# Kernel optimization log

Measured on AMD Instinct MI355X. Metric: run time of the kernel, lower is better.

## Reference

```python
import jax, jax.numpy as jnp
import numpy as np

N = 100000       # nodes
E = 800000       # edges (avg degree 8)
D_IN = 256
D_H = 128
K = 16           # cluster_num
LAMBDA1 = 1.0    # args.alphaH
LAMBDA2 = 0.5    # args.alphaO
GAMMA = 0.1      # args.step_size_gamma


def setup_inputs() -> dict:
    key = jax.random.key(0)
    ks = jax.random.split(key, 8)
    x = jax.random.normal(ks[0], (N, D_IN), jnp.float32)
    edge_index = jax.random.randint(ks[1], (2, E), 0, N, jnp.int32)
    # learned params (glorot-ish small init to keep Gram term numerically tame)
    W1 = jax.random.normal(ks[2], (D_IN, D_H), jnp.float32) * 0.002
    b1 = jnp.zeros((D_H,), jnp.float32)
    W2 = jax.random.normal(ks[3], (D_H, D_H), jnp.float32) * 0.01
    b2 = jnp.zeros((D_H,), jnp.float32)
    Wf = jax.random.normal(ks[4], (D_H, K), jnp.float32) * 0.05
    bf = jnp.zeros((K,), jnp.float32)
    return {"x": x, "edge_index": edge_index, "W1": W1, "b1": b1,
            "W2": W2, "b2": b2, "Wf": Wf, "bf": bf}


def _gcn_norm(edge_index, n):
    # add self loops, symmetric normalization D^-1/2 A D^-1/2 (PyG gcn_norm)
    loops = jnp.arange(n, dtype=edge_index.dtype)
    row = jnp.concatenate([edge_index[0], loops])   # source
    col = jnp.concatenate([edge_index[1], loops])   # target
    w = jnp.ones(row.shape[0], jnp.float32)
    deg = jax.ops.segment_sum(w, col, num_segments=n)
    dinv = jnp.where(deg > 0, jax.lax.rsqrt(jnp.maximum(deg, 1.0)), 0.0)
    return row, col, dinv[row] * w * dinv[col]


def _deprop_layer(x, W, b, row, col, w, n):
    x = x @ W                                               # lin (no bias)
    z = (1.0 - GAMMA * LAMBDA1 + GAMMA * LAMBDA2) * x
    # propagate: gather source features, scale by edge weight, scatter-add to target
    s = GAMMA * LAMBDA1 * jax.ops.segment_sum(w[:, None] * x[row], col, num_segments=n)
    # dense Gram correction: x @ (x^T x), d_h x d_h contraction
    t = GAMMA * LAMBDA2 * (x @ (x.T @ x))
    return jax.nn.relu(z + s - t + b)                       # bias add + ReLU


def reference(x, edge_index, W1, b1, W2, b2, Wf, bf):
    n = x.shape[0]
    row, col, w = _gcn_norm(edge_index, n)  # cached=True -> computed once, reused
    x = _deprop_layer(x, W1, b1, row, col, w, n)
    x = _deprop_layer(x, W2, b2, row, col, w, n)
    logits = x @ Wf + bf                    # fc; dropout is identity in eval mode
    return jax.nn.log_softmax(logits, axis=1)
```

## Files before the change

kernel.cpp:

```cpp
#include <hip/hip_runtime.h>

#define NNODES 100000
#define NEDGES 800000
#define DIN    256
#define DH     128
#define KCLS   16
#define SCAN_NBLK 98
#define GCH 64
#define GRAM_BLK 256

typedef unsigned short u16;
typedef short s16x8 __attribute__((ext_vector_type(8)));
typedef float f32x4 __attribute__((ext_vector_type(4)));

static constexpr float CZ = 0.95f;
static constexpr float CS = 0.10f;
static constexpr float CT = 0.05f;

__device__ __forceinline__ u16 f2b(float f) {
    unsigned u = __builtin_bit_cast(unsigned, f);
    return (u16)((u + 0x7FFFu + ((u >> 16) & 1u)) >> 16);
}
__device__ __forceinline__ float b2f(u16 b) {
    return __builtin_bit_cast(float, ((unsigned)b) << 16);
}


__global__ __launch_bounds__(256) void zero_kernel(int* __restrict__ p) {
    int i = blockIdx.x * 256 + threadIdx.x;
    if (i < NNODES) p[i] = 0;
}

__global__ __launch_bounds__(256) void hist_kernel(const int* __restrict__ col, int* counts) {
    int i = blockIdx.x * 256 + threadIdx.x;
    if (i < NEDGES) atomicAdd(&counts[col[i]], 1);
}

__global__ __launch_bounds__(256) void dinv_kernel(const int* __restrict__ counts, float* dinv) {
    int i = blockIdx.x * 256 + threadIdx.x;
    if (i < NNODES) dinv[i] = rsqrtf((float)(counts[i] + 1));
}

__global__ __launch_bounds__(256) void scan1_kernel(const int* __restrict__ counts,
                                                    int* __restrict__ offsets, int* __restrict__ bsum) {
    __shared__ int ls[256];
    const int b = blockIdx.x, t = threadIdx.x;
    const int base = b * 1024 + t * 4;
    int v0 = (base + 0 < NNODES) ? counts[base + 0] : 0;
    int v1 = (base + 1 < NNODES) ? counts[base + 1] : 0;
    int v2 = (base + 2 < NNODES) ? counts[base + 2] : 0;
    int v3 = (base + 3 < NNODES) ? counts[base + 3] : 0;
    ls[t] = v0 + v1 + v2 + v3;
    __syncthreads();
    for (int off = 1; off < 256; off <<= 1) {
        int v = (t >= off) ? ls[t - off] : 0;
        __syncthreads();
        ls[t] += v;
        __syncthreads();
    }
    int excl = (t == 0) ? 0 : ls[t - 1];
    if (t == 255) bsum[b] = ls[255];
    if (base + 0 < NNODES) offsets[base + 0] = excl;
    if (base + 1 < NNODES) offsets[base + 1] = excl + v0;
    if (base + 2 < NNODES) offsets[base + 2] = excl + v0 + v1;
    if (base + 3 < NNODES) offsets[base + 3] = excl + v0 + v1 + v2;
}

__global__ __launch_bounds__(128) void scan2_kernel(int* bsum) {
    __shared__ int ls[128];
    const int t = threadIdx.x;
    int v = (t < SCAN_NBLK) ? bsum[t] : 0;
    ls[t] = v;
    __syncthreads();
    for (int off = 1; off < 128; off <<= 1) {
        int u = (t >= off) ? ls[t - off] : 0;
        __syncthreads();
        ls[t] += u;
        __syncthreads();
    }
    if (t < SCAN_NBLK) bsum[t] = ls[t] - v;
}

__global__ __launch_bounds__(256) void scan3_kernel(int* __restrict__ offsets, const int* __restrict__ bsum) {
    const int b = blockIdx.x, t = threadIdx.x;
    const int add = bsum[b];
    const int base = b * 1024 + t * 4;
    #pragma unroll
    for (int i = 0; i < 4; ++i)
        if (base + i < NNODES) offsets[base + i] += add;
    if (b == 0 && t == 0) offsets[NNODES] = NEDGES;
}

__global__ __launch_bounds__(256)
void fill_kernel(const int* __restrict__ row, const int* __restrict__ col,
                 const int* __restrict__ offsets, int* __restrict__ cursor,
                 int* __restrict__ eidx) {
    int e = blockIdx.x * 256 + threadIdx.x;
    if (e >= NEDGES) return;
    int c = col[e];
    int p = offsets[c] + atomicAdd(&cursor[c], 1);
    eidx[p] = row[e];
}

__global__ __launch_bounds__(256)
void gather_b(const u16* __restrict__ Hb, const float* __restrict__ dinv,
              const int* __restrict__ offsets, const int* __restrict__ eidx,
              u16* __restrict__ Sb) {
    const int t = threadIdx.x;
    const int grp = t >> 4;
    const int gl  = t & 15;
    const int node = blockIdx.x * 16 + grp;
    if (node >= NNODES) return;
    const s16x8* H8 = (const s16x8*)Hb;
    const float d = dinv[node];
    s16x8 hv = H8[(size_t)node * 16 + gl];
    float a[8];
    #pragma unroll
    for (int i = 0; i < 8; ++i) a[i] = d * d * b2f((u16)hv[i]);
    int p = offsets[node];
    const int e = offsets[node + 1];
    for (; p + 1 < e; p += 2) {
        int   r0 = eidx[p],  r1 = eidx[p + 1];
        float w0 = dinv[r0] * d, w1 = dinv[r1] * d;
        s16x8 h0 = H8[(size_t)r0 * 16 + gl];
        s16x8 h1 = H8[(size_t)r1 * 16 + gl];
        #pragma unroll
        for (int i = 0; i < 8; ++i) a[i] = fmaf(w0, b2f((u16)h0[i]), a[i]);
        #pragma unroll
        for (int i = 0; i < 8; ++i) a[i] = fmaf(w1, b2f((u16)h1[i]), a[i]);
    }
    if (p < e) {
        int   r0 = eidx[p];
        float w0 = dinv[r0] * d;
        s16x8 h0 = H8[(size_t)r0 * 16 + gl];
        #pragma unroll
        for (int i = 0; i < 8; ++i) a[i] = fmaf(w0, b2f((u16)h0[i]), a[i]);
    }
    s16x8 o;
    #pragma unroll
    for (int i = 0; i < 8; ++i) o[i] = (short)f2b(a[i]);
    ((s16x8*)Sb)[(size_t)node * 16 + gl] = o;
}


__global__ __launch_bounds__(256)
void cvt_x_kernel(const float* __restrict__ x, u16* __restrict__ xb) {
    const long total = (long)NNODES * DIN / 8;
    for (long i = blockIdx.x * 256L + threadIdx.x; i < total; i += (long)gridDim.x * 256) {
        const float4* p = (const float4*)&x[i * 8];
        float4 u0 = p[0], u1 = p[1];
        s16x8 v;
        v[0] = (short)f2b(u0.x); v[1] = (short)f2b(u0.y);
        v[2] = (short)f2b(u0.z); v[3] = (short)f2b(u0.w);
        v[4] = (short)f2b(u1.x); v[5] = (short)f2b(u1.y);
        v[6] = (short)f2b(u1.z); v[7] = (short)f2b(u1.w);
        *(s16x8*)&xb[i * 8] = v;
    }
}

template<int KD>
__global__ __launch_bounds__(256)
void tr_w_kernel(const float* __restrict__ W, u16* __restrict__ Wt) {
    int idx = blockIdx.x * 256 + threadIdx.x;
    if (idx < 128 * KD) {
        int c = idx / KD, k = idx % KD;
        Wt[idx] = f2b(W[k * 128 + c]);
    }
}

template<int KD, int EPI>
__global__ __launch_bounds__(256, 4)
void mm_bt(const u16* __restrict__ A, const u16* __restrict__ Bt,
           u16* __restrict__ Out, const u16* __restrict__ Hb,
           const u16* __restrict__ Sb, const float* __restrict__ bias,
           int nrows)
{
    __shared__ __align__(16) u16 as_[2][128 * 40];
    __shared__ __align__(16) u16 bs_[2][128 * 40];
    const int t = threadIdx.x;
    const int w = t >> 6, l = t & 63;
    const int l15 = l & 15, g = l >> 4;
    const int row0 = blockIdx.x * 128;

    const int sr = t >> 2, so = t & 3;
    int arow[2];
    arow[0] = min(row0 + sr,      nrows - 1);
    arow[1] = min(row0 + 64 + sr, nrows - 1);

    #pragma unroll
    for (int i = 0; i < 2; ++i) {
        s16x8 va = *(const s16x8*)&A [(size_t)arow[i] * KD + so * 8];
        s16x8 vb = *(const s16x8*)&Bt[(size_t)(sr + i * 64) * KD + so * 8];
        *(s16x8*)&as_[0][(sr + i * 64) * 40 + so * 8] = va;
        *(s16x8*)&bs_[0][(sr + i * 64) * 40 + so * 8] = vb;
    }
    __syncthreads();

    f32x4 acc[2][8] = {};
    constexpr int NK = KD / 32;

    for (int kc = 0; kc < NK; ++kc) {
        const int buf = kc & 1;
        s16x8 va[2], vb[2];
        const bool pf = (kc + 1 < NK);
        if (pf) {
            const int k0 = (kc + 1) * 32;
            #pragma unroll
            for (int i = 0; i < 2; ++i) {
                va[i] = *(const s16x8*)&A [(size_t)arow[i] * KD + k0 + so * 8];
                vb[i] = *(const s16x8*)&Bt[(size_t)(sr + i * 64) * KD + k0 + so * 8];
            }
        }
        s16x8 af0 = *(const s16x8*)&as_[buf][(w * 32 +      l15) * 40 + g * 8];
        s16x8 af1 = *(const s16x8*)&as_[buf][(w * 32 + 16 + l15) * 40 + g * 8];
        #pragma unroll
        for (int n = 0; n < 8; ++n) {
            s16x8 bfr = *(const s16x8*)&bs_[buf][(n * 16 + l15) * 40 + g * 8];
            acc[0][n] = __builtin_amdgcn_mfma_f32_16x16x32_bf16(af0, bfr, acc[0][n], 0, 0, 0);
            acc[1][n] = __builtin_amdgcn_mfma_f32_16x16x32_bf16(af1, bfr, acc[1][n], 0, 0, 0);
        }
        if (pf) {
            #pragma unroll
            for (int i = 0; i < 2; ++i) {
                *(s16x8*)&as_[buf ^ 1][(sr + i * 64) * 40 + so * 8] = va[i];
                *(s16x8*)&bs_[buf ^ 1][(sr + i * 64) * 40 + so * 8] = vb[i];
            }
        }
        __syncthreads();
    }

    float bv[8];
    if (EPI) {
        #pragma unroll
        for (int n = 0; n < 8; ++n) bv[n] = bias[n * 16 + l15];
    }
    #pragma unroll
    for (int m = 0; m < 2; ++m) {
        #pragma unroll
        for (int j = 0; j < 4; ++j) {
            int grow = row0 + w * 32 + m * 16 + g * 4 + j;
            if (grow < nrows) {
                size_t base = (size_t)grow * 128;
                #pragma unroll
                for (int n = 0; n < 8; ++n) {
                    int col = n * 16 + l15;
                    float v = acc[m][n][j];
                    if (EPI) {
                        float h = b2f(Hb[base + col]);
                        float s = b2f(Sb[base + col]);
                        v = fmaxf(CZ * h + CS * s - CT * v + bv[n], 0.f);
                    }
                    Out[base + col] = f2b(v);
                }
            }
        }
    }
}

__global__ __launch_bounds__(256)
void gram_mfma(const u16* __restrict__ Hb, float* __restrict__ P, int nrows)
{
    __shared__ __align__(16) u16 ht[2][128 * GCH];
    const int t = threadIdx.x;
    const int w = t >> 6, l = t & 63;
    const int l15 = l & 15, g = l >> 4;
    const int nch = (nrows + GCH - 1) / GCH;

    f32x4 acc[2][8] = {};

    const int sr = t >> 2, sq = t & 3;

    {
        int gr = blockIdx.x * GCH + sr;
        #pragma unroll
        for (int i4 = 0; i4 < 4; ++i4) {
            int c0 = sq * 32 + i4 * 8;
            s16x8 v = {};
            if (gr < nrows) v = *(const s16x8*)&Hb[(size_t)gr * DH + c0];
            #pragma unroll
            for (int i = 0; i < 8; ++i) {
                int c = c0 + i;
                ht[0][c * GCH + (sr ^ ((c & 7) << 3))] = (u16)v[i];
            }
        }
    }
    __syncthreads();

    int buf = 0;
    for (int ch = blockIdx.x; ch < nch; ch += gridDim.x, buf ^= 1) {
        int chn = ch + gridDim.x;
        if (chn < nch) {
            int gr = chn * GCH + sr;
            #pragma unroll
            for (int i4 = 0; i4 < 4; ++i4) {
                int c0 = sq * 32 + i4 * 8;
                s16x8 v = {};
                if (gr < nrows) v = *(const s16x8*)&Hb[(size_t)gr * DH + c0];
                #pragma unroll
                for (int i = 0; i < 8; ++i) {
                    int c = c0 + i;
                    ht[buf ^ 1][c * GCH + (sr ^ ((c & 7) << 3))] = (u16)v[i];
                }
            }
        }
        #pragma unroll
        for (int ks = 0; ks < 2; ++ks) {
            const int kx = (ks * 32 + g * 8) ^ ((l & 7) << 3);
            s16x8 a0 = *(const s16x8*)&ht[buf][(w * 32 +      l15) * GCH + kx];
            s16x8 a1 = *(const s16x8*)&ht[buf][(w * 32 + 16 + l15) * GCH + kx];
            #pragma unroll
            for (int n = 0; n < 8; ++n) {
                s16x8 bfr = *(const s16x8*)&ht[buf][(n * 16 + l15) * GCH + kx];
                acc[0][n] = __builtin_amdgcn_mfma_f32_16x16x32_bf16(a0, bfr, acc[0][n], 0, 0, 0);
                acc[1][n] = __builtin_amdgcn_mfma_f32_16x16x32_bf16(a1, bfr, acc[1][n], 0, 0, 0);
            }
        }
        __syncthreads();
    }

    float* Pb = P + (size_t)blockIdx.x * (DH * DH);
    #pragma unroll
    for (int m = 0; m < 2; ++m)
        #pragma unroll
        for (int j = 0; j < 4; ++j) {
            int prow = w * 32 + m * 16 + g * 4 + j;
            #pragma unroll
            for (int n = 0; n < 8; ++n)
                Pb[prow * DH + n * 16 + l15] = acc[m][n][j];
        }
}

__global__ __launch_bounds__(256)
void gram_reduce(const float* __restrict__ P, u16* __restrict__ Gb) {
    int idx = blockIdx.x * 256 + threadIdx.x;
    float s = 0.f;
    #pragma unroll 8
    for (int p = 0; p < GRAM_BLK; ++p)
        s += P[(size_t)p * (DH * DH) + idx];
    Gb[idx] = f2b(s);
}

__global__ __launch_bounds__(256)
void fc_mfma(const u16* __restrict__ Xb, const float* __restrict__ Wf,
             const float* __restrict__ bf, float* __restrict__ out, int nrows)
{
    __shared__ __align__(16) u16 wt[KCLS * DH];
    const int t = threadIdx.x;
    const int w = t >> 6, l = t & 63;
    const int l15 = l & 15, g = l >> 4;
    const int row0 = blockIdx.x * 128 + w * 32;

    for (int idx = t; idx < KCLS * DH; idx += 256) {
        int c = idx >> 7, k = idx & 127;
        wt[c * DH + (k ^ ((c & 7) << 3))] = f2b(Wf[k * KCLS + c]);
    }
    __syncthreads();

    int r[2];
    r[0] = min(row0 + l15,      nrows - 1);
    r[1] = min(row0 + 16 + l15, nrows - 1);

    f32x4 acc[2] = {};
    #pragma unroll
    for (int k0 = 0; k0 < DH; k0 += 32) {
        s16x8 a0 = *(const s16x8*)&Xb[(size_t)r[0] * DH + k0 + g * 8];
        s16x8 a1 = *(const s16x8*)&Xb[(size_t)r[1] * DH + k0 + g * 8];
        s16x8 bfr = *(const s16x8*)&wt[l15 * DH + ((k0 + g * 8) ^ ((l & 7) << 3))];
        acc[0] = __builtin_amdgcn_mfma_f32_16x16x32_bf16(a0, bfr, acc[0], 0, 0, 0);
        acc[1] = __builtin_amdgcn_mfma_f32_16x16x32_bf16(a1, bfr, acc[1], 0, 0, 0);
    }

    const float bias = bf[l15];
    #pragma unroll
    for (int m = 0; m < 2; ++m) {
        #pragma unroll
        for (int j = 0; j < 4; ++j) {
            int grow = row0 + m * 16 + g * 4 + j;
            float v = acc[m][j] + bias;
            float mx = v;
            #pragma unroll
            for (int o = 8; o >= 1; o >>= 1)
                mx = fmaxf(mx, __shfl_xor(mx, o));
            float e = expf(v - mx);
            float ssum = e;
            #pragma unroll
            for (int o = 8; o >= 1; o >>= 1)
                ssum += __shfl_xor(ssum, o);
            if (grow < nrows)
                out[(size_t)grow * KCLS + l15] = v - mx - logf(ssum);
        }
    }
}

extern "C" void kernel_launch(void* const* d_in, const int* in_sizes, int n_in,
                              void* d_out, int out_size, void* d_ws, size_t ws_size,
                              hipStream_t stream) {
    const float* x  = (const float*)d_in[0];
    const int*   ei = (const int*)d_in[1];
    const float* W1 = (const float*)d_in[2];
    const float* b1 = (const float*)d_in[3];
    const float* W2 = (const float*)d_in[4];
    const float* b2 = (const float*)d_in[5];
    const float* Wf = (const float*)d_in[6];
    const float* bf = (const float*)d_in[7];
    float* out = (float*)d_out;

    const int* row = ei;
    const int* col = ei + NEDGES;

    float* dinv    = (float*)d_ws;
    float* P       = dinv + 102400;
    int*   counts  = (int*)(P + (size_t)GRAM_BLK * DH * DH);
    int*   offsets = counts + 102400;
    int*   bsum    = offsets + 102656;
    int*   eidx    = bsum + 128;
    u16*   B0b     = (u16*)(eidx + NEDGES);
    u16*   xb      = B0b + (size_t)NNODES * DH;
    u16*   B1b     = xb;
    u16*   Sb      = xb + (size_t)NNODES * DH;
    u16*   W1t     = xb + (size_t)NNODES * DIN;
    u16*   W2t     = W1t + 128 * DIN;
    u16*   Gb      = W2t + 128 * DH;

    dim3 b256(256);
    const int gN  = (NNODES + 255) / 256;
    const int gE  = (NEDGES + 255) / 256;
    const int gMM = (NNODES + 127) / 128;
    const int gGA = (NNODES + 15) / 16;

    zero_kernel<<<gN, b256, 0, stream>>>(counts);
    hist_kernel<<<gE, b256, 0, stream>>>(col, counts);
    dinv_kernel<<<gN, b256, 0, stream>>>(counts, dinv);
    scan1_kernel<<<SCAN_NBLK, b256, 0, stream>>>(counts, offsets, bsum);
    scan2_kernel<<<1, 128, 0, stream>>>(bsum);
    scan3_kernel<<<SCAN_NBLK, b256, 0, stream>>>(offsets, bsum);
    zero_kernel<<<gN, b256, 0, stream>>>(counts);
    fill_kernel<<<gE, b256, 0, stream>>>(row, col, offsets, counts, eidx);
    cvt_x_kernel<<<2048, b256, 0, stream>>>(x, xb);
    tr_w_kernel<DIN><<<(128 * DIN + 255) / 256, b256, 0, stream>>>(W1, W1t);
    tr_w_kernel<DH><<<(128 * DH + 255) / 256, b256, 0, stream>>>(W2, W2t);

    mm_bt<DIN, 0><<<gMM, b256, 0, stream>>>(xb, W1t, B0b, nullptr, nullptr, nullptr, NNODES);
    gram_mfma<<<GRAM_BLK, b256, 0, stream>>>(B0b, P, NNODES);
    gram_reduce<<<64, b256, 0, stream>>>(P, Gb);
    gather_b<<<gGA, b256, 0, stream>>>(B0b, dinv, offsets, eidx, Sb);
    mm_bt<DH, 1><<<gMM, b256, 0, stream>>>(B0b, Gb, B1b, B0b, Sb, b1, NNODES);

    mm_bt<DH, 0><<<gMM, b256, 0, stream>>>(B1b, W2t, B0b, nullptr, nullptr, nullptr, NNODES);
    gram_mfma<<<GRAM_BLK, b256, 0, stream>>>(B0b, P, NNODES);
    gram_reduce<<<64, b256, 0, stream>>>(P, Gb);
    gather_b<<<gGA, b256, 0, stream>>>(B0b, dinv, offsets, eidx, Sb);
    mm_bt<DH, 1><<<gMM, b256, 0, stream>>>(B0b, Gb, B1b, B0b, Sb, b2, NNODES);

    fc_mfma<<<gMM, b256, 0, stream>>>(B1b, Wf, bf, out, NNODES);
}
```

Before: 334.0 us.

## Fuse fp32-to-bf16 conversion into first GEMM and co-launch Gram with gather

The standalone cvt_x pass is removed, so the first mm_bt reads fp32 x directly and converts it to bf16 while loading tiles. This avoids writing and re-reading a bf16 copy of x, at the price of twice the bytes per A-tile load inside the GEMM. The Gram partial-product kernel and the neighbour gather kernel are also merged into one launch, with the first 256 blocks doing Gram and the rest doing gather. This lets the two independent stages run side by side and fill the GPU, but it makes the block types within one kernel uneven in work. Workspace buffers are relaid out now that xb is gone.

```diff
diff --git a/kernel.cpp b/kernel.cpp
--- a/kernel.cpp
+++ b/kernel.cpp
@@ -23,6 +23,14 @@
 }
 __device__ __forceinline__ float b2f(u16 b) {
     return __builtin_bit_cast(float, ((unsigned)b) << 16);
+}
+__device__ __forceinline__ s16x8 f2b8(float4 u0, float4 u1) {
+    s16x8 v;
+    v[0] = (short)f2b(u0.x); v[1] = (short)f2b(u0.y);
+    v[2] = (short)f2b(u0.z); v[3] = (short)f2b(u0.w);
+    v[4] = (short)f2b(u1.x); v[5] = (short)f2b(u1.y);
+    v[6] = (short)f2b(u1.z); v[7] = (short)f2b(u1.w);
+    return v;
 }
 
 
@@ -102,61 +110,6 @@
     eidx[p] = row[e];
 }
 
-__global__ __launch_bounds__(256)
-void gather_b(const u16* __restrict__ Hb, const float* __restrict__ dinv,
-              const int* __restrict__ offsets, const int* __restrict__ eidx,
-              u16* __restrict__ Sb) {
-    const int t = threadIdx.x;
-    const int grp = t >> 4;
-    const int gl  = t & 15;
-    const int node = blockIdx.x * 16 + grp;
-    if (node >= NNODES) return;
-    const s16x8* H8 = (const s16x8*)Hb;
-    const float d = dinv[node];
-    s16x8 hv = H8[(size_t)node * 16 + gl];
-    float a[8];
-    #pragma unroll
-    for (int i = 0; i < 8; ++i) a[i] = d * d * b2f((u16)hv[i]);
-    int p = offsets[node];
-    const int e = offsets[node + 1];
-    for (; p + 1 < e; p += 2) {
-        int   r0 = eidx[p],  r1 = eidx[p + 1];
-        float w0 = dinv[r0] * d, w1 = dinv[r1] * d;
-        s16x8 h0 = H8[(size_t)r0 * 16 + gl];
-        s16x8 h1 = H8[(size_t)r1 * 16 + gl];
-        #pragma unroll
-        for (int i = 0; i < 8; ++i) a[i] = fmaf(w0, b2f((u16)h0[i]), a[i]);
-        #pragma unroll
-        for (int i = 0; i < 8; ++i) a[i] = fmaf(w1, b2f((u16)h1[i]), a[i]);
-    }
-    if (p < e) {
-        int   r0 = eidx[p];
-        float w0 = dinv[r0] * d;
-        s16x8 h0 = H8[(size_t)r0 * 16 + gl];
-        #pragma unroll
-        for (int i = 0; i < 8; ++i) a[i] = fmaf(w0, b2f((u16)h0[i]), a[i]);
-    }
-    s16x8 o;
-    #pragma unroll
-    for (int i = 0; i < 8; ++i) o[i] = (short)f2b(a[i]);
-    ((s16x8*)Sb)[(size_t)node * 16 + gl] = o;
-}
-
-
-__global__ __launch_bounds__(256)
-void cvt_x_kernel(const float* __restrict__ x, u16* __restrict__ xb) {
-    const long total = (long)NNODES * DIN / 8;
-    for (long i = blockIdx.x * 256L + threadIdx.x; i < total; i += (long)gridDim.x * 256) {
-        const float4* p = (const float4*)&x[i * 8];
-        float4 u0 = p[0], u1 = p[1];
-        s16x8 v;
-        v[0] = (short)f2b(u0.x); v[1] = (short)f2b(u0.y);
-        v[2] = (short)f2b(u0.z); v[3] = (short)f2b(u0.w);
-        v[4] = (short)f2b(u1.x); v[5] = (short)f2b(u1.y);
-        v[6] = (short)f2b(u1.z); v[7] = (short)f2b(u1.w);
-        *(s16x8*)&xb[i * 8] = v;
-    }
-}
 
 template<int KD>
 __global__ __launch_bounds__(256)
@@ -168,9 +121,9 @@
     }
 }
 
-template<int KD, int EPI>
+template<int KD, int EPI, int AF>
 __global__ __launch_bounds__(256, 4)
-void mm_bt(const u16* __restrict__ A, const u16* __restrict__ Bt,
+void mm_bt(const void* __restrict__ Avoid, const u16* __restrict__ Bt,
            u16* __restrict__ Out, const u16* __restrict__ Hb,
            const u16* __restrict__ Sb, const float* __restrict__ bias,
            int nrows)
@@ -182,6 +135,9 @@
     const int l15 = l & 15, g = l >> 4;
     const int row0 = blockIdx.x * 128;
 
+    const u16*   Ab = (const u16*)Avoid;
+    const float* Af = (const float*)Avoid;
+
     const int sr = t >> 2, so = t & 3;
     int arow[2];
     arow[0] = min(row0 + sr,      nrows - 1);
@@ -189,7 +145,13 @@
 
     #pragma unroll
     for (int i = 0; i < 2; ++i) {
-        s16x8 va = *(const s16x8*)&A [(size_t)arow[i] * KD + so * 8];
+        s16x8 va;
+        if (AF) {
+            const float4* p = (const float4*)&Af[(size_t)arow[i] * KD + so * 8];
+            va = f2b8(p[0], p[1]);
+        } else {
+            va = *(const s16x8*)&Ab[(size_t)arow[i] * KD + so * 8];
+        }
         s16x8 vb = *(const s16x8*)&Bt[(size_t)(sr + i * 64) * KD + so * 8];
         *(s16x8*)&as_[0][(sr + i * 64) * 40 + so * 8] = va;
         *(s16x8*)&bs_[0][(sr + i * 64) * 40 + so * 8] = vb;
@@ -207,7 +169,12 @@
             const int k0 = (kc + 1) * 32;
             #pragma unroll
             for (int i = 0; i < 2; ++i) {
-                va[i] = *(const s16x8*)&A [(size_t)arow[i] * KD + k0 + so * 8];
+                if (AF) {
+                    const float4* p = (const float4*)&Af[(size_t)arow[i] * KD + k0 + so * 8];
+                    va[i] = f2b8(p[0], p[1]);
+                } else {
+                    va[i] = *(const s16x8*)&Ab[(size_t)arow[i] * KD + k0 + so * 8];
+                }
                 vb[i] = *(const s16x8*)&Bt[(size_t)(sr + i * 64) * KD + k0 + so * 8];
             }
         }
@@ -258,39 +225,24 @@
 }
 
 __global__ __launch_bounds__(256)
-void gram_mfma(const u16* __restrict__ Hb, float* __restrict__ P, int nrows)
+void gram_gather(const u16* __restrict__ Hb, const float* __restrict__ dinv,
+                 const int* __restrict__ offsets, const int* __restrict__ eidx,
+                 float* __restrict__ P, u16* __restrict__ Sb, int nrows)
 {
     __shared__ __align__(16) u16 ht[2][128 * GCH];
     const int t = threadIdx.x;
-    const int w = t >> 6, l = t & 63;
-    const int l15 = l & 15, g = l >> 4;
-    const int nch = (nrows + GCH - 1) / GCH;
-
-    f32x4 acc[2][8] = {};
-
-    const int sr = t >> 2, sq = t & 3;
-
-    {
-        int gr = blockIdx.x * GCH + sr;
-        #pragma unroll
-        for (int i4 = 0; i4 < 4; ++i4) {
-            int c0 = sq * 32 + i4 * 8;
-            s16x8 v = {};
-            if (gr < nrows) v = *(const s16x8*)&Hb[(size_t)gr * DH + c0];
-            #pragma unroll
-            for (int i = 0; i < 8; ++i) {
-                int c = c0 + i;
-                ht[0][c * GCH + (sr ^ ((c & 7) << 3))] = (u16)v[i];
-            }
-        }
-    }
-    __syncthreads();
-
-    int buf = 0;
-    for (int ch = blockIdx.x; ch < nch; ch += gridDim.x, buf ^= 1) {
-        int chn = ch + gridDim.x;
-        if (chn < nch) {
-            int gr = chn * GCH + sr;
+
+    if (blockIdx.x < GRAM_BLK) {
+        const int bid = blockIdx.x;
+        const int w = t >> 6, l = t & 63;
+        const int l15 = l & 15, g = l >> 4;
+        const int nch = (nrows + GCH - 1) / GCH;
+
+        f32x4 acc[2][8] = {};
+        const int sr = t >> 2, sq = t & 3;
+
+        {
+            int gr = bid * GCH + sr;
             #pragma unroll
             for (int i4 = 0; i4 < 4; ++i4) {
                 int c0 = sq * 32 + i4 * 8;
@@ -299,35 +251,89 @@
                 #pragma unroll
                 for (int i = 0; i < 8; ++i) {
                     int c = c0 + i;
-                    ht[buf ^ 1][c * GCH + (sr ^ ((c & 7) << 3))] = (u16)v[i];
+                    ht[0][c * GCH + (sr ^ ((c & 7) << 3))] = (u16)v[i];
                 }
             }
         }
-        #pragma unroll
-        for (int ks = 0; ks < 2; ++ks) {
-            const int kx = (ks * 32 + g * 8) ^ ((l & 7) << 3);
-            s16x8 a0 = *(const s16x8*)&ht[buf][(w * 32 +      l15) * GCH + kx];
-            s16x8 a1 = *(const s16x8*)&ht[buf][(w * 32 + 16 + l15) * GCH + kx];
-            #pragma unroll
-            for (int n = 0; n < 8; ++n) {
-                s16x8 bfr = *(const s16x8*)&ht[buf][(n * 16 + l15) * GCH + kx];
-                acc[0][n] = __builtin_amdgcn_mfma_f32_16x16x32_bf16(a0, bfr, acc[0][n], 0, 0, 0);
-                acc[1][n] = __builtin_amdgcn_mfma_f32_16x16x32_bf16(a1, bfr, acc[1][n], 0, 0, 0);
-            }
-        }
-        __syncthreads();
-    }
-
-    float* Pb = P + (size_t)blockIdx.x * (DH * DH);
-    #pragma unroll
-    for (int m = 0; m < 2; ++m)
-        #pragma unroll
-        for (int j = 0; j < 4; ++j) {
-            int prow = w * 32 + m * 16 + g * 4 + j;
-            #pragma unroll
-            for (int n = 0; n < 8; ++n)
-                Pb[prow * DH + n * 16 + l15] = acc[m][n][j];
-        }
+        __syncthreads();
+
+        int buf = 0;
+        for (int ch = bid; ch < nch; ch += GRAM_BLK, buf ^= 1) {
+            int chn = ch + GRAM_BLK;
+            if (chn < nch) {
+                int gr = chn * GCH + sr;
+                #pragma unroll
+                for (int i4 = 0; i4 < 4; ++i4) {
+                    int c0 = sq * 32 + i4 * 8;
+                    s16x8 v = {};
+                    if (gr < nrows) v = *(const s16x8*)&Hb[(size_t)gr * DH + c0];
+                    #pragma unroll
+                    for (int i = 0; i < 8; ++i) {
+                        int c = c0 + i;
+                        ht[buf ^ 1][c * GCH + (sr ^ ((c & 7) << 3))] = (u16)v[i];
+                    }
+                }
+            }
+            #pragma unroll
+            for (int ks = 0; ks < 2; ++ks) {
+                const int kx = (ks * 32 + g * 8) ^ ((l & 7) << 3);
+                s16x8 a0 = *(const s16x8*)&ht[buf][(w * 32 +      l15) * GCH + kx];
+                s16x8 a1 = *(const s16x8*)&ht[buf][(w * 32 + 16 + l15) * GCH + kx];
+                #pragma unroll
+                for (int n = 0; n < 8; ++n) {
+                    s16x8 bfr = *(const s16x8*)&ht[buf][(n * 16 + l15) * GCH + kx];
+                    acc[0][n] = __builtin_amdgcn_mfma_f32_16x16x32_bf16(a0, bfr, acc[0][n], 0, 0, 0);
+                    acc[1][n] = __builtin_amdgcn_mfma_f32_16x16x32_bf16(a1, bfr, acc[1][n], 0, 0, 0);
+                }
+            }
+            __syncthreads();
+        }
+
+        float* Pb = P + (size_t)bid * (DH * DH);
+        #pragma unroll
+        for (int m = 0; m < 2; ++m)
+            #pragma unroll
+            for (int j = 0; j < 4; ++j) {
+                int prow = w * 32 + m * 16 + g * 4 + j;
+                #pragma unroll
+                for (int n = 0; n < 8; ++n)
+                    Pb[prow * DH + n * 16 + l15] = acc[m][n][j];
+            }
+    } else {
+        const int grp = t >> 4;
+        const int gl  = t & 15;
+        const int node = (blockIdx.x - GRAM_BLK) * 16 + grp;
+        if (node >= NNODES) return;
+        const s16x8* H8 = (const s16x8*)Hb;
+        const float d = dinv[node];
+        s16x8 hv = H8[(size_t)node * 16 + gl];
+        float a[8];
+        #pragma unroll
+        for (int i = 0; i < 8; ++i) a[i] = d * d * b2f((u16)hv[i]);
+        int p = offsets[node];
+        const int e = offsets[node + 1];
+        for (; p + 1 < e; p += 2) {
+            int   r0 = eidx[p],  r1 = eidx[p + 1];
+            float w0 = dinv[r0] * d, w1 = dinv[r1] * d;
+            s16x8 h0 = H8[(size_t)r0 * 16 + gl];
+            s16x8 h1 = H8[(size_t)r1 * 16 + gl];
+            #pragma unroll
+            for (int i = 0; i < 8; ++i) a[i] = fmaf(w0, b2f((u16)h0[i]), a[i]);
+            #pragma unroll
+            for (int i = 0; i < 8; ++i) a[i] = fmaf(w1, b2f((u16)h1[i]), a[i]);
+        }
+        if (p < e) {
+            int   r0 = eidx[p];
+            float w0 = dinv[r0] * d;
+            s16x8 h0 = H8[(size_t)r0 * 16 + gl];
+            #pragma unroll
+            for (int i = 0; i < 8; ++i) a[i] = fmaf(w0, b2f((u16)h0[i]), a[i]);
+        }
+        s16x8 o;
+        #pragma unroll
+        for (int i = 0; i < 8; ++i) o[i] = (short)f2b(a[i]);
+        ((s16x8*)Sb)[(size_t)node * 16 + gl] = o;
+    }
 }
 
 __global__ __launch_bounds__(256)
@@ -415,10 +421,9 @@
     int*   bsum    = offsets + 102656;
     int*   eidx    = bsum + 128;
     u16*   B0b     = (u16*)(eidx + NEDGES);
-    u16*   xb      = B0b + (size_t)NNODES * DH;
-    u16*   B1b     = xb;
-    u16*   Sb      = xb + (size_t)NNODES * DH;
-    u16*   W1t     = xb + (size_t)NNODES * DIN;
+    u16*   B1b     = B0b + (size_t)NNODES * DH;
+    u16*   Sb      = B1b + (size_t)NNODES * DH;
+    u16*   W1t     = Sb + (size_t)NNODES * DH;
     u16*   W2t     = W1t + 128 * DIN;
     u16*   Gb      = W2t + 128 * DH;
 
@@ -426,7 +431,7 @@
     const int gN  = (NNODES + 255) / 256;
     const int gE  = (NEDGES + 255) / 256;
     const int gMM = (NNODES + 127) / 128;
-    const int gGA = (NNODES + 15) / 16;
+    const int gGG = GRAM_BLK + (NNODES + 15) / 16;
 
     zero_kernel<<<gN, b256, 0, stream>>>(counts);
     hist_kernel<<<gE, b256, 0, stream>>>(col, counts);
@@ -436,21 +441,18 @@
     scan3_kernel<<<SCAN_NBLK, b256, 0, stream>>>(offsets, bsum);
     zero_kernel<<<gN, b256, 0, stream>>>(counts);
     fill_kernel<<<gE, b256, 0, stream>>>(row, col, offsets, counts, eidx);
-    cvt_x_kernel<<<2048, b256, 0, stream>>>(x, xb);
     tr_w_kernel<DIN><<<(128 * DIN + 255) / 256, b256, 0, stream>>>(W1, W1t);
     tr_w_kernel<DH><<<(128 * DH + 255) / 256, b256, 0, stream>>>(W2, W2t);
 
-    mm_bt<DIN, 0><<<gMM, b256, 0, stream>>>(xb, W1t, B0b, nullptr, nullptr, nullptr, NNODES);
-    gram_mfma<<<GRAM_BLK, b256, 0, stream>>>(B0b, P, NNODES);
+    mm_bt<DIN, 0, 1><<<gMM, b256, 0, stream>>>(x, W1t, B0b, nullptr, nullptr, nullptr, NNODES);
+    gram_gather<<<gGG, b256, 0, stream>>>(B0b, dinv, offsets, eidx, P, Sb, NNODES);
     gram_reduce<<<64, b256, 0, stream>>>(P, Gb);
-    gather_b<<<gGA, b256, 0, stream>>>(B0b, dinv, offsets, eidx, Sb);
-    mm_bt<DH, 1><<<gMM, b256, 0, stream>>>(B0b, Gb, B1b, B0b, Sb, b1, NNODES);
-
-    mm_bt<DH, 0><<<gMM, b256, 0, stream>>>(B1b, W2t, B0b, nullptr, nullptr, nullptr, NNODES);
-    gram_mfma<<<GRAM_BLK, b256, 0, stream>>>(B0b, P, NNODES);
+    mm_bt<DH, 1, 0><<<gMM, b256, 0, stream>>>(B0b, Gb, B1b, B0b, Sb, b1, NNODES);
+
+    mm_bt<DH, 0, 0><<<gMM, b256, 0, stream>>>(B1b, W2t, B0b, nullptr, nullptr, nullptr, NNODES);
+    gram_gather<<<gGG, b256, 0, stream>>>(B0b, dinv, offsets, eidx, P, Sb, NNODES);
     gram_reduce<<<64, b256, 0, stream>>>(P, Gb);
-    gather_b<<<gGA, b256, 0, stream>>>(B0b, dinv, offsets, eidx, Sb);
-    mm_bt<DH, 1><<<gMM, b256, 0, stream>>>(B0b, Gb, B1b, B0b, Sb, b2, NNODES);
+    mm_bt<DH, 1, 0><<<gMM, b256, 0, stream>>>(B0b, Gb, B1b, B0b, Sb, b2, NNODES);
 
     fc_mfma<<<gMM, b256, 0, stream>>>(B1b, Wf, bf, out, NNODES);
 }
```

Result: no change. 333.6 us (-0.1%).
